# Kernel tuning notes

Measured on AMD Instinct MI355X. Metric: run time of the kernel, lower is better.

The kernel has to match this reference:

```python
import jax, jax.numpy as jnp
import numpy as np

N_QUBITS = 10
Q_DEPTH = 6
MAX_LAYERS = 15
DIM = 2 ** N_QUBITS


def _apply_1q(s, U, w):
    # s: (B, 2^n) real statevector (circuit uses only H/RY/CNOT, all real).
    # Wire 0 is the most-significant bit (PennyLane convention).
    a, b = 2 ** w, 2 ** (N_QUBITS - 1 - w)
    s = s.reshape(-1, a, 2, b)
    if U.ndim == 2:  # gate shared across batch
        s = jnp.einsum('ij,Bajb->Baib', U, s)
    else:            # per-sample gate, U: (B,2,2)
        s = jnp.einsum('Bij,Bajb->Baib', U, s)
    return s.reshape(-1, DIM)


def _apply_cnot(s, c, t):
    # CNOT, control c < target t
    s = s.reshape(-1, 2 ** c, 2, 2 ** (t - c - 1), 2, 2 ** (N_QUBITS - 1 - t))
    s = jnp.stack([s[:, :, 0], jnp.flip(s[:, :, 1], axis=3)], axis=2)
    return s.reshape(-1, DIM)


def _ry(theta):
    # RY(theta) = [[cos t/2, -sin t/2], [sin t/2, cos t/2]]; theta scalar or (B,)
    c, si = jnp.cos(theta / 2.0), jnp.sin(theta / 2.0)
    return jnp.stack([jnp.stack([c, -si], -1), jnp.stack([si, c], -1)], -2)


def _quantum_net(q_in, q_params):
    # q_in: (B, n_qubits) rotation angles; q_params: (max_layers*n_qubits,)
    B = q_in.shape[0]
    qw = q_params.reshape(MAX_LAYERS, N_QUBITS)
    s = jnp.zeros((B, DIM), q_in.dtype).at[:, 0].set(1.0)  # |0...0>
    H = jnp.array([[1.0, 1.0], [1.0, -1.0]], q_in.dtype) / jnp.sqrt(jnp.asarray(2.0, q_in.dtype))
    for w in range(N_QUBITS):
        s = _apply_1q(s, H, w)
    for w in range(N_QUBITS):
        s = _apply_1q(s, _ry(q_in[:, w]), w)
    for k in range(Q_DEPTH):
        for i in range(0, N_QUBITS - 1, 2):
            s = _apply_cnot(s, i, i + 1)
        for i in range(1, N_QUBITS - 1, 2):
            s = _apply_cnot(s, i, i + 1)
        for w in range(N_QUBITS):
            s = _apply_1q(s, _ry(qw[k + 1, w]), w)
    probs = s * s
    # <Z_w> = P(bit_w = 0) - P(bit_w = 1)
    z = []
    for w in range(N_QUBITS):
        p = probs.reshape(-1, 2 ** w, 2, 2 ** (N_QUBITS - 1 - w)).sum(axis=(1, 3))
        z.append(p[:, 0] - p[:, 1])
    return jnp.stack(z, axis=1)  # (B, n_qubits)


def setup_inputs() -> dict:
    key = jax.random.key(0)
    ks = jax.random.split(key, 6)
    B, F, NQ, NC = 8192, 512, N_QUBITS, 2
    q_delta = 0.01
    return {
        'input_features': jax.random.normal(ks[0], (B, F), jnp.float32),
        'W_pre': jax.random.normal(ks[1], (NQ, F), jnp.float32) / np.sqrt(F),
        'b_pre': jnp.zeros((NQ,), jnp.float32),
        'q_params': q_delta * jax.random.normal(ks[2], (MAX_LAYERS * NQ,), jnp.float32),
        'W_post': jax.random.normal(ks[3], (NC, NQ), jnp.float32) / np.sqrt(NQ),
        'b_post': jnp.zeros((NC,), jnp.float32),
    }


def reference(input_features, W_pre, b_pre, q_params, W_post, b_post):
    pre_out = input_features @ W_pre.T + b_pre          # (B, n_qubits)
    q_in = jnp.tanh(pre_out) * (np.pi / 2.0)            # scale to [-pi/2, pi/2]
    q_out = _quantum_net(q_in, q_params)                # (B, n_qubits) PauliZ expvals
    return q_out @ W_post.T + b_post                    # (B, n_classes)
```

## Files before the change

### kernel.cpp

```cpp
#include <hip/hip_runtime.h>
#include <math.h>


#define NQ   10
#define NREG 16
#define DIM  1024

typedef _Float16 f16;
typedef _Float16 f16x8 __attribute__((ext_vector_type(8)));
typedef float    f32x4 __attribute__((ext_vector_type(4)));

template<int BB>
__device__ __forceinline__ void ry_lane(float (&s)[NREG], int lane, float c, float si) {
    float sgn = ((lane >> BB) & 1) ? si : -si;
    #pragma unroll
    for (int r = 0; r < NREG; ++r) {
        float o = __shfl_xor(s[r], 1 << BB);
        s[r] = fmaf(sgn, o, c * s[r]);
    }
}
template<int P>
__device__ __forceinline__ void ry_reg(float (&s)[NREG], float c, float si) {
    const int m = 1 << P;
    #pragma unroll
    for (int r = 0; r < NREG; ++r) {
        if ((r & m) == 0) {
            float a = s[r], b = s[r + m];
            s[r]     = fmaf(c, a, -si * b);
            s[r + m] = fmaf(si, a,  c * b);
        }
    }
}
__device__ __forceinline__ void cnot_5_6(float (&s)[NREG], int lane) {
    bool sel = (lane & 1) != 0;
    #pragma unroll
    for (int r = 0; r < 8; ++r) {
        float a = s[r], b = s[r + 8];
        s[r]     = sel ? b : a;
        s[r + 8] = sel ? a : b;
    }
}
template<int PC, int PT>
__device__ __forceinline__ void cnot_reg(float (&s)[NREG]) {
    #pragma unroll
    for (int r = 0; r < NREG; ++r) {
        if (((r >> PC) & 1) && !((r >> PT) & 1)) {
            float t = s[r];
            s[r] = s[r ^ (1 << PT)];
            s[r ^ (1 << PT)] = t;
        }
    }
}
__device__ __forceinline__ void perm_even(float (&s)[NREG], int lane) {
    int src = lane ^ (((((lane >> 5) & 1) << 4)) | ((((lane >> 3) & 1) << 2)) | (((lane >> 1) & 1)));
    #pragma unroll
    for (int r = 0; r < NREG; ++r) s[r] = __shfl(s[r], src);
}
__device__ __forceinline__ void perm_odd(float (&s)[NREG], int lane) {
    int src = lane ^ (((((lane >> 4) & 1) << 3)) | ((((lane >> 2) & 1) << 1)));
    #pragma unroll
    for (int r = 0; r < NREG; ++r) s[r] = __shfl(s[r], src);
}

#define APPLY_RY_ALL(CARR, SARR, BASE)                                        \
    { float c_, s_;                                                           \
      c_=__shfl(CARR,(BASE)+0); s_=__shfl(SARR,(BASE)+0); ry_lane<5>(s,lane,c_,s_); \
      c_=__shfl(CARR,(BASE)+1); s_=__shfl(SARR,(BASE)+1); ry_lane<4>(s,lane,c_,s_); \
      c_=__shfl(CARR,(BASE)+2); s_=__shfl(SARR,(BASE)+2); ry_lane<3>(s,lane,c_,s_); \
      c_=__shfl(CARR,(BASE)+3); s_=__shfl(SARR,(BASE)+3); ry_lane<2>(s,lane,c_,s_); \
      c_=__shfl(CARR,(BASE)+4); s_=__shfl(SARR,(BASE)+4); ry_lane<1>(s,lane,c_,s_); \
      c_=__shfl(CARR,(BASE)+5); s_=__shfl(SARR,(BASE)+5); ry_lane<0>(s,lane,c_,s_); \
      c_=__shfl(CARR,(BASE)+6); s_=__shfl(SARR,(BASE)+6); ry_reg<3>(s,c_,s_);       \
      c_=__shfl(CARR,(BASE)+7); s_=__shfl(SARR,(BASE)+7); ry_reg<2>(s,c_,s_);       \
      c_=__shfl(CARR,(BASE)+8); s_=__shfl(SARR,(BASE)+8); ry_reg<1>(s,c_,s_);       \
      c_=__shfl(CARR,(BASE)+9); s_=__shfl(SARR,(BASE)+9); ry_reg<0>(s,c_,s_); }

__global__ __launch_bounds__(256) void k1_psi0(
    const float* __restrict__ X, const float* __restrict__ Wpre,
    const float* __restrict__ bpre, f16* __restrict__ psi0, int B)
{
    const int lane = threadIdx.x & 63;
    const int wave = threadIdx.x >> 6;
    const int sample = blockIdx.x * 4 + wave;
    if (sample >= B) return;

    const float* xrow = X + (size_t)sample * 512;
    float4 x0 = ((const float4*)xrow)[lane];
    float4 x1 = ((const float4*)xrow)[64 + lane];
    float acc[NQ];
    #pragma unroll
    for (int q = 0; q < NQ; ++q) {
        const float* wr = Wpre + q * 512;
        float4 w0 = ((const float4*)wr)[lane];
        float4 w1 = ((const float4*)wr)[64 + lane];
        float a = x0.x * w0.x;
        a = fmaf(x0.y, w0.y, a); a = fmaf(x0.z, w0.z, a); a = fmaf(x0.w, w0.w, a);
        a = fmaf(x1.x, w1.x, a); a = fmaf(x1.y, w1.y, a);
        a = fmaf(x1.z, w1.z, a); a = fmaf(x1.w, w1.w, a);
        acc[q] = a;
    }
    #pragma unroll
    for (int q = 0; q < NQ; ++q) {
        float v = acc[q];
        #pragma unroll
        for (int d = 32; d >= 1; d >>= 1) v += __shfl_xor(v, d);
        acc[q] = v;
    }
    float pre = acc[0];
    #pragma unroll
    for (int q = 1; q < NQ; ++q) pre = (lane == q) ? acc[q] : pre;

    float c45 = 0.0f, s45 = 0.0f;
    if (lane < NQ) {
        float th = tanhf(pre + bpre[lane]) * 1.5707963267948966f;
        sincosf(0.5f * th + 0.7853981633974483f, &s45, &c45);
    }

    float lv = 1.0f;
    #pragma unroll
    for (int w = 0; w < 6; ++w) {
        float f0 = __shfl(c45, w), f1 = __shfl(s45, w);
        lv *= ((lane >> (5 - w)) & 1) ? f1 : f0;
    }
    float c6 = __shfl(c45, 6), s6 = __shfl(s45, 6);
    float c7 = __shfl(c45, 7), s7 = __shfl(s45, 7);
    float c8 = __shfl(c45, 8), s8 = __shfl(s45, 8);
    float c9 = __shfl(c45, 9), s9 = __shfl(s45, 9);
    float g01[4] = {c6 * c7, c6 * s7, s6 * c7, s6 * s7};
    float g23[4] = {c8 * c9, c8 * s9, s8 * c9, s8 * s9};

    union { f16 h[16]; float4 v[2]; } u;
    #pragma unroll
    for (int r = 0; r < NREG; ++r)
        u.h[r] = (f16)(lv * g01[r >> 2] * g23[r & 3]);
    float4* dst = (float4*)((char*)psi0 + (size_t)sample * 2048 + lane * 32);
    dst[0] = u.v[0];
    dst[1] = u.v[1];
}

__global__ __launch_bounds__(256) void k2_arows(
    const float* __restrict__ qp, f16* __restrict__ Arm)
{
    const int lane = threadIdx.x & 63;
    const int wave = threadIdx.x >> 6;
    const int row = blockIdx.x * 4 + wave;

    float cw = 1.0f, swn = 0.0f;
    if (lane < 60) {
        float s_, c_;
        sincosf(0.5f * qp[10 + lane], &s_, &c_);
        cw = c_; swn = -s_;
    }

    float s[NREG];
    int srcLane = row >> 4, srcReg = row & 15;
    #pragma unroll
    for (int r = 0; r < NREG; ++r)
        s[r] = (lane == srcLane && r == srcReg) ? 1.0f : 0.0f;

    for (int kk = 6; kk >= 1; --kk) {
        APPLY_RY_ALL(cw, swn, (kk - 1) * 10);
        perm_odd(s, lane);
        cnot_5_6(s, lane);
        cnot_reg<2, 1>(s);
        perm_even(s, lane);
        cnot_reg<3, 2>(s);
        cnot_reg<1, 0>(s);
    }

    union { f16 h[16]; float4 v[2]; } u;
    #pragma unroll
    for (int r = 0; r < NREG; ++r) u.h[r] = (f16)s[r];
    float4* dst = (float4*)((char*)Arm + (size_t)row * 2048 + lane * 32);
    dst[0] = u.v[0];
    dst[1] = u.v[1];
}

__device__ __forceinline__ void async16(const void* g, void* l) {
    __builtin_amdgcn_global_load_lds(
        (const __attribute__((address_space(1))) void*)g,
        (__attribute__((address_space(3))) void*)l, 16, 0, 0);
}

__global__ __launch_bounds__(256) void k3_gemm(
    const f16* __restrict__ P0, const f16* __restrict__ Arm, f16* __restrict__ Pf)
{
    __shared__ f16 As[128 * 32];
    __shared__ f16 Bs[128 * 32];
    const int tid = threadIdx.x, lane = tid & 63;
    const int wv = tid >> 6;
    const int wm = (wv >> 1) * 64, wn = (wv & 1) * 64;
    const size_t tM = (size_t)blockIdx.x * 128, tN = (size_t)blockIdx.y * 128;

    f32x4 acc[4][4] = {};

    const int c0 = tid, c1 = tid + 256;
    const int r0 = c0 >> 2, o0 = (c0 & 3) * 8;
    const int r1 = c1 >> 2, o1 = (c1 & 3) * 8;
    const f16* gA0 = P0 + (tM + r0) * 1024 + o0;
    const f16* gA1 = P0 + (tM + r1) * 1024 + o1;
    const f16* gB0 = Arm + (tN + r0) * 1024 + o0;
    const f16* gB1 = Arm + (tN + r1) * 1024 + o1;

    const int aoff = (lane & 15) * 32 + (lane >> 4) * 8;
    const f16* Af = As + wm * 32 + aoff;
    const f16* Bf = Bs + wn * 32 + aoff;

    for (int kt = 0; kt < 1024; kt += 32) {
        async16(gA0 + kt, As + c0 * 8);
        async16(gA1 + kt, As + c1 * 8);
        async16(gB0 + kt, Bs + c0 * 8);
        async16(gB1 + kt, Bs + c1 * 8);
        __syncthreads();
        f16x8 af[4], bf[4];
        #pragma unroll
        for (int i = 0; i < 4; ++i) af[i] = *(const f16x8*)(Af + i * 512);
        #pragma unroll
        for (int j = 0; j < 4; ++j) bf[j] = *(const f16x8*)(Bf + j * 512);
        #pragma unroll
        for (int i = 0; i < 4; ++i)
            #pragma unroll
            for (int j = 0; j < 4; ++j)
                acc[i][j] = __builtin_amdgcn_mfma_f32_16x16x32_f16(af[i], bf[j], acc[i][j], 0, 0, 0);
        __syncthreads();
    }

    const int cn = lane & 15, rq = (lane >> 4) * 4;
    #pragma unroll
    for (int i = 0; i < 4; ++i)
        #pragma unroll
        for (int t = 0; t < 4; ++t) {
            size_t m = tM + wm + i * 16 + rq + t;
            f16* dst = Pf + m * 1024 + tN + wn + cn;
            #pragma unroll
            for (int j = 0; j < 4; ++j) dst[j * 16] = (f16)acc[i][j][t];
        }
}

__global__ __launch_bounds__(256) void k4_measure(
    const f16* __restrict__ Pf, const float* __restrict__ Wpost,
    const float* __restrict__ bpost, float* __restrict__ out, int B)
{
    const int lane = threadIdx.x & 63;
    const int wave = threadIdx.x >> 6;
    const int sample = blockIdx.x * 4 + wave;
    if (sample >= B) return;

    union { f16 h[16]; float4 v[2]; } u;
    const float4* src = (const float4*)((const char*)Pf + (size_t)sample * 2048 + lane * 32);
    u.v[0] = src[0];
    u.v[1] = src[1];

    float p[NREG], tot = 0.0f;
    #pragma unroll
    for (int r = 0; r < NREG; ++r) { float a = (float)u.h[r]; p[r] = a * a; tot += p[r]; }

    float z[NQ];
    #pragma unroll
    for (int w = 0; w < 6; ++w) {
        int b = 5 - w;
        z[w] = ((lane >> b) & 1) ? -tot : tot;
    }
    z[6] = z[7] = z[8] = z[9] = 0.0f;
    #pragma unroll
    for (int r = 0; r < NREG; ++r) {
        z[6] += ((r >> 3) & 1) ? -p[r] : p[r];
        z[7] += ((r >> 2) & 1) ? -p[r] : p[r];
        z[8] += ((r >> 1) & 1) ? -p[r] : p[r];
        z[9] += ((r >> 0) & 1) ? -p[r] : p[r];
    }
    #pragma unroll
    for (int w = 0; w < NQ; ++w) {
        float v = z[w];
        #pragma unroll
        for (int d = 32; d >= 1; d >>= 1) v += __shfl_xor(v, d);
        z[w] = v;
    }
    if (lane < 2) {
        const float* wp = Wpost + lane * NQ;
        float o = bpost[lane];
        #pragma unroll
        for (int w = 0; w < NQ; ++w) o = fmaf(z[w], wp[w], o);
        out[(size_t)sample * 2 + lane] = o;
    }
}

template<int BC, int BT>
__device__ __forceinline__ void cnot_lane(float (&s)[NREG], int lane) {
    int src = ((lane >> BC) & 1) ? (lane ^ (1 << BT)) : lane;
    #pragma unroll
    for (int r = 0; r < NREG; ++r) s[r] = __shfl(s[r], src);
}

__global__ __launch_bounds__(256) void hybrid_head_fallback(
    const float* __restrict__ X, const float* __restrict__ Wpre,
    const float* __restrict__ bpre, const float* __restrict__ qp,
    const float* __restrict__ Wpost, const float* __restrict__ bpost,
    float* __restrict__ out, int B)
{
    const int lane = threadIdx.x & 63;
    const int wave = threadIdx.x >> 6;
    const int sample = blockIdx.x * 4 + wave;
    if (sample >= B) return;

    const float* xrow = X + (size_t)sample * 512;
    float4 x0 = ((const float4*)xrow)[lane];
    float4 x1 = ((const float4*)xrow)[64 + lane];
    float acc[NQ];
    #pragma unroll
    for (int q = 0; q < NQ; ++q) {
        const float* wr = Wpre + q * 512;
        float4 w0 = ((const float4*)wr)[lane];
        float4 w1 = ((const float4*)wr)[64 + lane];
        float a = x0.x * w0.x;
        a = fmaf(x0.y, w0.y, a); a = fmaf(x0.z, w0.z, a); a = fmaf(x0.w, w0.w, a);
        a = fmaf(x1.x, w1.x, a); a = fmaf(x1.y, w1.y, a);
        a = fmaf(x1.z, w1.z, a); a = fmaf(x1.w, w1.w, a);
        acc[q] = a;
    }
    #pragma unroll
    for (int q = 0; q < NQ; ++q) {
        float v = acc[q];
        #pragma unroll
        for (int d = 32; d >= 1; d >>= 1) v += __shfl_xor(v, d);
        acc[q] = v;
    }
    float pre = acc[0];
    #pragma unroll
    for (int q = 1; q < NQ; ++q) pre = (lane == q) ? acc[q] : pre;
    float cth = 1.0f, sth = 0.0f;
    if (lane < NQ) {
        float th = tanhf(pre + bpre[lane]) * 1.5707963267948966f;
        sincosf(0.5f * th, &sth, &cth);
    }
    float cw = 1.0f, sw = 0.0f;
    if (lane < 60) sincosf(0.5f * qp[10 + lane], &sw, &cw);

    float s[NREG];
    #pragma unroll
    for (int r = 0; r < NREG; ++r) s[r] = 0.03125f;
    APPLY_RY_ALL(cth, sth, 0);
    for (int k = 0; k < 6; ++k) {
        perm_even(s, lane);
        cnot_reg<3, 2>(s);
        cnot_reg<1, 0>(s);
        perm_odd(s, lane);
        cnot_5_6(s, lane);
        cnot_reg<2, 1>(s);
        APPLY_RY_ALL(cw, sw, k * 10);
    }
    float p[NREG], tot = 0.0f;
    #pragma unroll
    for (int r = 0; r < NREG; ++r) { p[r] = s[r] * s[r]; tot += p[r]; }
    float z[NQ];
    #pragma unroll
    for (int w = 0; w < 6; ++w) z[w] = ((lane >> (5 - w)) & 1) ? -tot : tot;
    z[6] = z[7] = z[8] = z[9] = 0.0f;
    #pragma unroll
    for (int r = 0; r < NREG; ++r) {
        z[6] += ((r >> 3) & 1) ? -p[r] : p[r];
        z[7] += ((r >> 2) & 1) ? -p[r] : p[r];
        z[8] += ((r >> 1) & 1) ? -p[r] : p[r];
        z[9] += ((r >> 0) & 1) ? -p[r] : p[r];
    }
    #pragma unroll
    for (int w = 0; w < NQ; ++w) {
        float v = z[w];
        #pragma unroll
        for (int d = 32; d >= 1; d >>= 1) v += __shfl_xor(v, d);
        z[w] = v;
    }
    if (lane < 2) {
        const float* wp = Wpost + lane * NQ;
        float o = bpost[lane];
        #pragma unroll
        for (int w = 0; w < NQ; ++w) o = fmaf(z[w], wp[w], o);
        out[(size_t)sample * 2 + lane] = o;
    }
}

extern "C" void kernel_launch(void* const* d_in, const int* in_sizes, int n_in,
                              void* d_out, int out_size, void* d_ws, size_t ws_size,
                              hipStream_t stream) {
    const float* X     = (const float*)d_in[0];
    const float* Wpre  = (const float*)d_in[1];
    const float* bpre  = (const float*)d_in[2];
    const float* qp    = (const float*)d_in[3];
    const float* Wpost = (const float*)d_in[4];
    const float* bpost = (const float*)d_in[5];
    float* out = (float*)d_out;
    int B = in_sizes[0] / 512;

    size_t psi0_bytes = (size_t)B * DIM * sizeof(f16);
    size_t arm_bytes  = (size_t)DIM * DIM * sizeof(f16);
    size_t psif_bytes = (size_t)B * DIM * sizeof(f16);
    size_t need = psi0_bytes + arm_bytes + psif_bytes;

    if (ws_size < need) {
        hipLaunchKernelGGL(hybrid_head_fallback, dim3((B + 3) / 4), dim3(256), 0, stream,
                           X, Wpre, bpre, qp, Wpost, bpost, out, B);
        return;
    }

    char* ws = (char*)d_ws;
    f16* psi0 = (f16*)ws;
    f16* Arm  = (f16*)(ws + psi0_bytes);
    f16* psif = (f16*)(ws + psi0_bytes + arm_bytes);

    hipLaunchKernelGGL(k1_psi0, dim3((B + 3) / 4), dim3(256), 0, stream, X, Wpre, bpre, psi0, B);
    hipLaunchKernelGGL(k2_arows, dim3(DIM / 4), dim3(256), 0, stream, qp, Arm);
    hipLaunchKernelGGL(k3_gemm, dim3(B / 128, DIM / 128), dim3(256), 0, stream, psi0, Arm, psif);
    hipLaunchKernelGGL(k4_measure, dim3((B + 3) / 4), dim3(256), 0, stream, psif, Wpost, bpost, out, B);
}
```

Baseline: 129.9 us.

## Fuse measurement into GEMM epilogue and merge prep kernels into one

Merges the psi0 and A-row preparation kernels into a single launch. Folds the Z-expectation reduction into the GEMM epilogue, so the final statevector is never written back in fp16. The GEMM now uses K-tiles of 64 with an XOR-swizzled LDS layout to avoid bank conflicts. Per-N-tile partial Z sums are stored in a small buffer and reduced by a tiny post kernel. This cuts global traffic and launch count, at the cost of a hardcoded B=8192 path and more complex epilogue shuffles.

```diff
diff --git a/kernel.cpp b/kernel.cpp
--- a/kernel.cpp
+++ b/kernel.cpp
@@ -75,214 +75,242 @@
       c_=__shfl(CARR,(BASE)+8); s_=__shfl(SARR,(BASE)+8); ry_reg<1>(s,c_,s_);       \
       c_=__shfl(CARR,(BASE)+9); s_=__shfl(SARR,(BASE)+9); ry_reg<0>(s,c_,s_); }
 
-__global__ __launch_bounds__(256) void k1_psi0(
-    const float* __restrict__ X, const float* __restrict__ Wpre,
-    const float* __restrict__ bpre, f16* __restrict__ psi0, int B)
-{
-    const int lane = threadIdx.x & 63;
-    const int wave = threadIdx.x >> 6;
-    const int sample = blockIdx.x * 4 + wave;
-    if (sample >= B) return;
-
-    const float* xrow = X + (size_t)sample * 512;
-    float4 x0 = ((const float4*)xrow)[lane];
-    float4 x1 = ((const float4*)xrow)[64 + lane];
-    float acc[NQ];
-    #pragma unroll
-    for (int q = 0; q < NQ; ++q) {
-        const float* wr = Wpre + q * 512;
-        float4 w0 = ((const float4*)wr)[lane];
-        float4 w1 = ((const float4*)wr)[64 + lane];
-        float a = x0.x * w0.x;
-        a = fmaf(x0.y, w0.y, a); a = fmaf(x0.z, w0.z, a); a = fmaf(x0.w, w0.w, a);
-        a = fmaf(x1.x, w1.x, a); a = fmaf(x1.y, w1.y, a);
-        a = fmaf(x1.z, w1.z, a); a = fmaf(x1.w, w1.w, a);
-        acc[q] = a;
-    }
-    #pragma unroll
-    for (int q = 0; q < NQ; ++q) {
-        float v = acc[q];
-        #pragma unroll
-        for (int d = 32; d >= 1; d >>= 1) v += __shfl_xor(v, d);
-        acc[q] = v;
-    }
-    float pre = acc[0];
-    #pragma unroll
-    for (int q = 1; q < NQ; ++q) pre = (lane == q) ? acc[q] : pre;
-
-    float c45 = 0.0f, s45 = 0.0f;
-    if (lane < NQ) {
-        float th = tanhf(pre + bpre[lane]) * 1.5707963267948966f;
-        sincosf(0.5f * th + 0.7853981633974483f, &s45, &c45);
-    }
-
-    float lv = 1.0f;
-    #pragma unroll
-    for (int w = 0; w < 6; ++w) {
-        float f0 = __shfl(c45, w), f1 = __shfl(s45, w);
-        lv *= ((lane >> (5 - w)) & 1) ? f1 : f0;
-    }
-    float c6 = __shfl(c45, 6), s6 = __shfl(s45, 6);
-    float c7 = __shfl(c45, 7), s7 = __shfl(s45, 7);
-    float c8 = __shfl(c45, 8), s8 = __shfl(s45, 8);
-    float c9 = __shfl(c45, 9), s9 = __shfl(s45, 9);
-    float g01[4] = {c6 * c7, c6 * s7, s6 * c7, s6 * s7};
-    float g23[4] = {c8 * c9, c8 * s9, s8 * c9, s8 * s9};
-
-    union { f16 h[16]; float4 v[2]; } u;
-    #pragma unroll
-    for (int r = 0; r < NREG; ++r)
-        u.h[r] = (f16)(lv * g01[r >> 2] * g23[r & 3]);
-    float4* dst = (float4*)((char*)psi0 + (size_t)sample * 2048 + lane * 32);
-    dst[0] = u.v[0];
-    dst[1] = u.v[1];
-}
-
-__global__ __launch_bounds__(256) void k2_arows(
-    const float* __restrict__ qp, f16* __restrict__ Arm)
-{
-    const int lane = threadIdx.x & 63;
-    const int wave = threadIdx.x >> 6;
-    const int row = blockIdx.x * 4 + wave;
-
-    float cw = 1.0f, swn = 0.0f;
-    if (lane < 60) {
-        float s_, c_;
-        sincosf(0.5f * qp[10 + lane], &s_, &c_);
-        cw = c_; swn = -s_;
-    }
-
-    float s[NREG];
-    int srcLane = row >> 4, srcReg = row & 15;
-    #pragma unroll
-    for (int r = 0; r < NREG; ++r)
-        s[r] = (lane == srcLane && r == srcReg) ? 1.0f : 0.0f;
-
-    for (int kk = 6; kk >= 1; --kk) {
-        APPLY_RY_ALL(cw, swn, (kk - 1) * 10);
-        perm_odd(s, lane);
-        cnot_5_6(s, lane);
-        cnot_reg<2, 1>(s);
-        perm_even(s, lane);
-        cnot_reg<3, 2>(s);
-        cnot_reg<1, 0>(s);
-    }
-
-    union { f16 h[16]; float4 v[2]; } u;
-    #pragma unroll
-    for (int r = 0; r < NREG; ++r) u.h[r] = (f16)s[r];
-    float4* dst = (float4*)((char*)Arm + (size_t)row * 2048 + lane * 32);
-    dst[0] = u.v[0];
-    dst[1] = u.v[1];
-}
-
 __device__ __forceinline__ void async16(const void* g, void* l) {
     __builtin_amdgcn_global_load_lds(
         (const __attribute__((address_space(1))) void*)g,
         (__attribute__((address_space(3))) void*)l, 16, 0, 0);
 }
 
-__global__ __launch_bounds__(256) void k3_gemm(
-    const f16* __restrict__ P0, const f16* __restrict__ Arm, f16* __restrict__ Pf)
+__global__ __launch_bounds__(256) void ka_prepare(
+    const float* __restrict__ X, const float* __restrict__ Wpre,
+    const float* __restrict__ bpre, const float* __restrict__ qp,
+    f16* __restrict__ psi0, f16* __restrict__ Arm, int B)
 {
-    __shared__ f16 As[128 * 32];
-    __shared__ f16 Bs[128 * 32];
-    const int tid = threadIdx.x, lane = tid & 63;
-    const int wv = tid >> 6;
+    const int tid = threadIdx.x, lane = tid & 63, wv = tid >> 6;
+
+    for (int it = 0; it < 4; ++it) {
+        int sample = blockIdx.x * 16 + wv * 4 + it;
+        if (sample >= B) break;
+        const float* xrow = X + (size_t)sample * 512;
+        float4 x0 = ((const float4*)xrow)[lane];
+        float4 x1 = ((const float4*)xrow)[64 + lane];
+        float acc[NQ];
+        #pragma unroll
+        for (int q = 0; q < NQ; ++q) {
+            const float* wr = Wpre + q * 512;
+            float4 w0 = ((const float4*)wr)[lane];
+            float4 w1 = ((const float4*)wr)[64 + lane];
+            float a = x0.x * w0.x;
+            a = fmaf(x0.y, w0.y, a); a = fmaf(x0.z, w0.z, a); a = fmaf(x0.w, w0.w, a);
+            a = fmaf(x1.x, w1.x, a); a = fmaf(x1.y, w1.y, a);
+            a = fmaf(x1.z, w1.z, a); a = fmaf(x1.w, w1.w, a);
+            acc[q] = a;
+        }
+        #pragma unroll
+        for (int q = 0; q < NQ; ++q) {
+            float v = acc[q];
+            #pragma unroll
+            for (int d = 32; d >= 1; d >>= 1) v += __shfl_xor(v, d);
+            acc[q] = v;
+        }
+        float pre = acc[0];
+        #pragma unroll
+        for (int q = 1; q < NQ; ++q) pre = (lane == q) ? acc[q] : pre;
+        float c45 = 0.0f, s45 = 0.0f;
+        if (lane < NQ) {
+            float th = tanhf(pre + bpre[lane]) * 1.5707963267948966f;
+            sincosf(0.5f * th + 0.7853981633974483f, &s45, &c45);
+        }
+        float lv = 1.0f;
+        #pragma unroll
+        for (int w = 0; w < 6; ++w) {
+            float f0 = __shfl(c45, w), f1 = __shfl(s45, w);
+            lv *= ((lane >> (5 - w)) & 1) ? f1 : f0;
+        }
+        float c6 = __shfl(c45, 6), s6 = __shfl(s45, 6);
+        float c7 = __shfl(c45, 7), s7 = __shfl(s45, 7);
+        float c8 = __shfl(c45, 8), s8 = __shfl(s45, 8);
+        float c9 = __shfl(c45, 9), s9 = __shfl(s45, 9);
+        float g01[4] = {c6 * c7, c6 * s7, s6 * c7, s6 * s7};
+        float g23[4] = {c8 * c9, c8 * s9, s8 * c9, s8 * s9};
+        union { f16 h[16]; float4 v[2]; } u;
+        #pragma unroll
+        for (int r = 0; r < NREG; ++r)
+            u.h[r] = (f16)(lv * g01[r >> 2] * g23[r & 3]);
+        float4* dst = (float4*)((char*)psi0 + (size_t)sample * 2048 + lane * 32);
+        dst[0] = u.v[0];
+        dst[1] = u.v[1];
+    }
+
+    if (wv < 2) {
+        int row = blockIdx.x * 2 + wv;
+        if (row < DIM) {
+            float cw = 1.0f, swn = 0.0f;
+            if (lane < 60) {
+                float s_, c_;
+                sincosf(0.5f * qp[10 + lane], &s_, &c_);
+                cw = c_; swn = -s_;
+            }
+            float s[NREG];
+            int srcLane = row >> 4, srcReg = row & 15;
+            #pragma unroll
+            for (int r = 0; r < NREG; ++r)
+                s[r] = (lane == srcLane && r == srcReg) ? 1.0f : 0.0f;
+            for (int kk = 6; kk >= 1; --kk) {
+                APPLY_RY_ALL(cw, swn, (kk - 1) * 10);
+                perm_odd(s, lane);
+                cnot_5_6(s, lane);
+                cnot_reg<2, 1>(s);
+                perm_even(s, lane);
+                cnot_reg<3, 2>(s);
+                cnot_reg<1, 0>(s);
+            }
+            union { f16 h[16]; float4 v[2]; } u;
+            #pragma unroll
+            for (int r = 0; r < NREG; ++r) u.h[r] = (f16)s[r];
+            float4* dst = (float4*)((char*)Arm + (size_t)row * 2048 + lane * 32);
+            dst[0] = u.v[0];
+            dst[1] = u.v[1];
+        }
+    }
+}
+
+__global__ __launch_bounds__(256, 2) void kb_gemm_measure(
+    const f16* __restrict__ psi0, const f16* __restrict__ Arm,
+    float* __restrict__ zpart)
+{
+    __shared__ __align__(16) char smem[32768];
+    const int tid = threadIdx.x, lane = tid & 63, wv = tid >> 6;
+
+    const int mB = blockIdx.x & 63, nB = blockIdx.x >> 6;
+    const size_t tM = (size_t)mB * 128, tN = (size_t)nB * 128;
+    f16* As = (f16*)smem;
+    f16* Bs = (f16*)(smem + 16384);
     const int wm = (wv >> 1) * 64, wn = (wv & 1) * 64;
-    const size_t tM = (size_t)blockIdx.x * 128, tN = (size_t)blockIdx.y * 128;
 
     f32x4 acc[4][4] = {};
 
-    const int c0 = tid, c1 = tid + 256;
-    const int r0 = c0 >> 2, o0 = (c0 & 3) * 8;
-    const int r1 = c1 >> 2, o1 = (c1 & 3) * 8;
-    const f16* gA0 = P0 + (tM + r0) * 1024 + o0;
-    const f16* gA1 = P0 + (tM + r1) * 1024 + o1;
-    const f16* gB0 = Arm + (tN + r0) * 1024 + o0;
-    const f16* gB1 = Arm + (tN + r1) * 1024 + o1;
-
-    const int aoff = (lane & 15) * 32 + (lane >> 4) * 8;
-    const f16* Af = As + wm * 32 + aoff;
-    const f16* Bf = Bs + wn * 32 + aoff;
-
-    for (int kt = 0; kt < 1024; kt += 32) {
-        async16(gA0 + kt, As + c0 * 8);
-        async16(gA1 + kt, As + c1 * 8);
-        async16(gB0 + kt, Bs + c0 * 8);
-        async16(gB1 + kt, Bs + c1 * 8);
+    const f16* ga[4]; const f16* gb[4]; int ldso[4];
+    #pragma unroll
+    for (int p = 0; p < 4; ++p) {
+        int slot = p * 256 + tid;
+        int row = slot >> 3, gp = slot & 7, g = gp ^ (row & 7);
+        ga[p] = psi0 + (tM + row) * 1024 + g * 8;
+        gb[p] = Arm  + (tN + row) * 1024 + g * 8;
+        ldso[p] = slot * 16;
+    }
+
+    for (int kt = 0; kt < 1024; kt += 64) {
         __syncthreads();
-        f16x8 af[4], bf[4];
-        #pragma unroll
-        for (int i = 0; i < 4; ++i) af[i] = *(const f16x8*)(Af + i * 512);
-        #pragma unroll
-        for (int j = 0; j < 4; ++j) bf[j] = *(const f16x8*)(Bf + j * 512);
-        #pragma unroll
-        for (int i = 0; i < 4; ++i)
-            #pragma unroll
-            for (int j = 0; j < 4; ++j)
-                acc[i][j] = __builtin_amdgcn_mfma_f32_16x16x32_f16(af[i], bf[j], acc[i][j], 0, 0, 0);
+        #pragma unroll
+        for (int p = 0; p < 4; ++p) async16(ga[p] + kt, (char*)As + ldso[p]);
+        #pragma unroll
+        for (int p = 0; p < 4; ++p) async16(gb[p] + kt, (char*)Bs + ldso[p]);
         __syncthreads();
-    }
-
-    const int cn = lane & 15, rq = (lane >> 4) * 4;
-    #pragma unroll
-    for (int i = 0; i < 4; ++i)
+        #pragma unroll
+        for (int ks = 0; ks < 2; ++ks) {
+            f16x8 af[4], bf[4];
+            const int gpb = ks * 4 + (lane >> 4);
+            const int gpx = gpb ^ (lane & 7);
+            #pragma unroll
+            for (int i = 0; i < 4; ++i) {
+                int rowA = wm + i * 16 + (lane & 15);
+                af[i] = *(const f16x8*)(As + rowA * 64 + gpx * 8);
+            }
+            #pragma unroll
+            for (int j = 0; j < 4; ++j) {
+                int rowB = wn + j * 16 + (lane & 15);
+                bf[j] = *(const f16x8*)(Bs + rowB * 64 + gpx * 8);
+            }
+            #pragma unroll
+            for (int i = 0; i < 4; ++i)
+                #pragma unroll
+                for (int j = 0; j < 4; ++j)
+                    acc[i][j] = __builtin_amdgcn_mfma_f32_16x16x32_f16(af[i], bf[j], acc[i][j], 0, 0, 0);
+        }
+    }
+
+    __syncthreads();
+    float* zb = (float*)smem + (wn ? 1280 : 0);
+    const float sg0 = (nB & 4) ? -1.0f : 1.0f;
+    const float sg1 = (nB & 2) ? -1.0f : 1.0f;
+    const float sg2 = (nB & 1) ? -1.0f : 1.0f;
+    const float sg3 = wn ? -1.0f : 1.0f;
+
+    #pragma unroll
+    for (int i = 0; i < 4; ++i) {
         #pragma unroll
         for (int t = 0; t < 4; ++t) {
-            size_t m = tM + wm + i * 16 + rq + t;
-            f16* dst = Pf + m * 1024 + tN + wn + cn;
-            #pragma unroll
-            for (int j = 0; j < 4; ++j) dst[j * 16] = (f16)acc[i][j][t];
-        }
-}
-
-__global__ __launch_bounds__(256) void k4_measure(
-    const f16* __restrict__ Pf, const float* __restrict__ Wpost,
+            float p0 = acc[i][0][t] * acc[i][0][t];
+            float p1 = acc[i][1][t] * acc[i][1][t];
+            float p2 = acc[i][2][t] * acc[i][2][t];
+            float p3 = acc[i][3][t] * acc[i][3][t];
+            float t0  = (p0 + p1) + (p2 + p3);
+            float tw5 = (p0 - p1) + (p2 - p3);
+            float tw4 = (p0 + p1) - (p2 + p3);
+            float s1 = __shfl_xor(t0, 1);
+            float Av = t0 + s1;
+            float Bv = (lane & 1) ? s1 - t0 : t0 - s1;
+            float sA = __shfl_xor(Av, 2), sB = __shfl_xor(Bv, 2);
+            float AP = Av + sA;
+            float AM = (lane & 2) ? sA - Av : Av - sA;
+            float BP = Bv + sB;
+            float sAP = __shfl_xor(AP, 4), sAM = __shfl_xor(AM, 4), sBP = __shfl_xor(BP, 4);
+            float APP = AP + sAP;
+            float APM = (lane & 4) ? sAP - AP : AP - sAP;
+            float AMP = AM + sAM;
+            float BPP = BP + sBP;
+            float a1 = __shfl_xor(APP, 8), a2 = __shfl_xor(APM, 8);
+            float a3 = __shfl_xor(AMP, 8), a4 = __shfl_xor(BPP, 8);
+            float T0 = APP + a1;
+            float S6 = (lane & 8) ? a1 - APP : APP - a1;
+            float S7 = APM + a2;
+            float S8 = AMP + a3;
+            float S9 = BPP + a4;
+            float T5 = tw5, T4 = tw4;
+            T5 += __shfl_xor(T5, 1); T5 += __shfl_xor(T5, 2);
+            T5 += __shfl_xor(T5, 4); T5 += __shfl_xor(T5, 8);
+            T4 += __shfl_xor(T4, 1); T4 += __shfl_xor(T4, 2);
+            T4 += __shfl_xor(T4, 4); T4 += __shfl_xor(T4, 8);
+            if ((lane & 15) == 0) {
+                int row = wm + i * 16 + (lane >> 4) * 4 + t;
+                float* d = zb + row * 10;
+                d[0] = sg0 * T0; d[1] = sg1 * T0; d[2] = sg2 * T0; d[3] = sg3 * T0;
+                d[4] = T4; d[5] = T5;
+                d[6] = S6; d[7] = S7; d[8] = S8; d[9] = S9;
+            }
+        }
+    }
+    __syncthreads();
+    float* zall = (float*)smem;
+    for (int idx = tid; idx < 1280; idx += 256) {
+        float v = zall[idx] + zall[1280 + idx];
+        int row = idx / 10, w = idx - row * 10;
+        zpart[((size_t)nB * 8192 + tM + row) * 10 + w] = v;
+    }
+}
+
+__global__ __launch_bounds__(256) void kc_post(
+    const float* __restrict__ zpart, const float* __restrict__ Wpost,
     const float* __restrict__ bpost, float* __restrict__ out, int B)
 {
-    const int lane = threadIdx.x & 63;
-    const int wave = threadIdx.x >> 6;
-    const int sample = blockIdx.x * 4 + wave;
-    if (sample >= B) return;
-
-    union { f16 h[16]; float4 v[2]; } u;
-    const float4* src = (const float4*)((const char*)Pf + (size_t)sample * 2048 + lane * 32);
-    u.v[0] = src[0];
-    u.v[1] = src[1];
-
-    float p[NREG], tot = 0.0f;
-    #pragma unroll
-    for (int r = 0; r < NREG; ++r) { float a = (float)u.h[r]; p[r] = a * a; tot += p[r]; }
-
-    float z[NQ];
-    #pragma unroll
-    for (int w = 0; w < 6; ++w) {
-        int b = 5 - w;
-        z[w] = ((lane >> b) & 1) ? -tot : tot;
-    }
-    z[6] = z[7] = z[8] = z[9] = 0.0f;
-    #pragma unroll
-    for (int r = 0; r < NREG; ++r) {
-        z[6] += ((r >> 3) & 1) ? -p[r] : p[r];
-        z[7] += ((r >> 2) & 1) ? -p[r] : p[r];
-        z[8] += ((r >> 1) & 1) ? -p[r] : p[r];
-        z[9] += ((r >> 0) & 1) ? -p[r] : p[r];
-    }
+    int gid = blockIdx.x * 256 + threadIdx.x;
+    if (gid >= B) return;
+    float z[NQ] = {};
+    #pragma unroll
+    for (int nb = 0; nb < 8; ++nb) {
+        const float* zp = zpart + ((size_t)nb * 8192 + gid) * 10;
+        #pragma unroll
+        for (int w = 0; w < NQ; ++w) z[w] += zp[w];
+    }
+    float o0 = bpost[0], o1 = bpost[1];
     #pragma unroll
     for (int w = 0; w < NQ; ++w) {
-        float v = z[w];
-        #pragma unroll
-        for (int d = 32; d >= 1; d >>= 1) v += __shfl_xor(v, d);
-        z[w] = v;
-    }
-    if (lane < 2) {
-        const float* wp = Wpost + lane * NQ;
-        float o = bpost[lane];
-        #pragma unroll
-        for (int w = 0; w < NQ; ++w) o = fmaf(z[w], wp[w], o);
-        out[(size_t)sample * 2 + lane] = o;
-    }
+        o0 = fmaf(z[w], Wpost[w], o0);
+        o1 = fmaf(z[w], Wpost[NQ + w], o1);
+    }
+    out[(size_t)gid * 2 + 0] = o0;
+    out[(size_t)gid * 2 + 1] = o1;
 }
 
 template<int BC, int BT>
@@ -391,24 +419,26 @@
     float* out = (float*)d_out;
     int B = in_sizes[0] / 512;
 
-    size_t psi0_bytes = (size_t)B * DIM * sizeof(f16);
-    size_t arm_bytes  = (size_t)DIM * DIM * sizeof(f16);
-    size_t psif_bytes = (size_t)B * DIM * sizeof(f16);
-    size_t need = psi0_bytes + arm_bytes + psif_bytes;
-
-    if (ws_size < need) {
+    size_t psi0_b  = (size_t)B * DIM * sizeof(f16);
+    size_t arm_b   = (size_t)DIM * DIM * sizeof(f16);
+    size_t zpart_b = (size_t)8 * 8192 * 10 * sizeof(float);
+    size_t need = psi0_b + arm_b + zpart_b;
+
+    if (B != 8192 || ws_size < need) {
         hipLaunchKernelGGL(hybrid_head_fallback, dim3((B + 3) / 4), dim3(256), 0, stream,
                            X, Wpre, bpre, qp, Wpost, bpost, out, B);
         return;
     }
 
     char* ws = (char*)d_ws;
-    f16* psi0 = (f16*)ws;
-    f16* Arm  = (f16*)(ws + psi0_bytes);
-    f16* psif = (f16*)(ws + psi0_bytes + arm_bytes);
-
-    hipLaunchKernelGGL(k1_psi0, dim3((B + 3) / 4), dim3(256), 0, stream, X, Wpre, bpre, psi0, B);
-    hipLaunchKernelGGL(k2_arows, dim3(DIM / 4), dim3(256), 0, stream, qp, Arm);
-    hipLaunchKernelGGL(k3_gemm, dim3(B / 128, DIM / 128), dim3(256), 0, stream, psi0, Arm, psif);
-    hipLaunchKernelGGL(k4_measure, dim3((B + 3) / 4), dim3(256), 0, stream, psif, Wpost, bpost, out, B);
-}
+    f16*   psi0  = (f16*)ws;
+    f16*   Arm   = (f16*)(ws + psi0_b);
+    float* zpart = (float*)(ws + psi0_b + arm_b);
+
+    hipLaunchKernelGGL(ka_prepare, dim3(512), dim3(256), 0, stream,
+                       X, Wpre, bpre, qp, psi0, Arm, B);
+    hipLaunchKernelGGL(kb_gemm_measure, dim3(512), dim3(256), 0, stream,
+                       psi0, Arm, zpart);
+    hipLaunchKernelGGL(kc_post, dim3(32), dim3(256), 0, stream,
+                       zpart, Wpost, bpost, out, B);
+}
```

New measurement: 126.2 us. 1.03x faster.
